# Kernel optimization log

Hardware: AMD Instinct MI355X
Metric: run time of the kernel (lower is better)

Reference implementation:

```python
import jax, jax.numpy as jnp
import numpy as np

D = 1024  # d_model

def setup_inputs() -> dict:
    key = jax.random.key(0)
    ks = jax.random.split(key, 12)
    s = 1.0 / np.sqrt(D)  # torch Linear default init scale
    inp = {
        "q": jax.random.normal(ks[0], (4, 4096, D), dtype=jnp.float32),
        "k": jax.random.normal(ks[1], (4, 4096, D), dtype=jnp.float32),
        "v": jax.random.normal(ks[2], (4, 4096, D), dtype=jnp.float32),
        "Wq": jax.random.uniform(ks[3], (D, D), jnp.float32, -s, s),
        "bq": jax.random.uniform(ks[4], (D,), jnp.float32, -s, s),
        "Wk": jax.random.uniform(ks[5], (D, D), jnp.float32, -s, s),
        "bk": jax.random.uniform(ks[6], (D,), jnp.float32, -s, s),
        "Wv": jax.random.uniform(ks[7], (D, D), jnp.float32, -s, s),
        "bv": jax.random.uniform(ks[8], (D,), jnp.float32, -s, s),
        "Wo": jax.random.uniform(ks[9], (D, D), jnp.float32, -s, s),
        "bo": jax.random.uniform(ks[10], (D,), jnp.float32, -s, s),
    }
    return inp

def reference(q, k, v, Wq, bq, Wk, bk, Wv, bv, Wo, bo):
    # phi feature map: exp(-x^2 / 2)
    phi = lambda x: jnp.exp(-0.5 * x * x)
    Q = phi(q @ Wq.T + bq)            # [B, N, D]
    K = phi(k @ Wk.T + bk)            # [B, N, D]
    V = v @ Wv.T + bv                 # [B, N, D]
    # linear attention: aggregate K^T V once, then contract with Q
    KV = jnp.einsum('bnd,bnl->bdl', K, V)                 # [B, D, D]
    Z = 1.0 / (jnp.einsum('bnd,bd->bn', Q, K.sum(axis=1)) + 1e-6)  # [B, N]
    out = jnp.einsum('bnd,bdl->bnl', Q, KV) * Z[..., None]         # [B, N, D]
    return out @ Wo.T + bo
```

## Files before the change

kernel.cpp:

```cpp
#include <hip/hip_runtime.h>

typedef unsigned short u16;
typedef unsigned int u32;
typedef unsigned long long u64;

typedef __attribute__((ext_vector_type(8))) short short8;
typedef __attribute__((ext_vector_type(4))) float floatx4;

__device__ __forceinline__ float b2f(u16 h) {
  u32 u = ((u32)h) << 16;
  return __builtin_bit_cast(float, u);
}
__device__ __forceinline__ u16 f2b(float f) {
  u32 u = __builtin_bit_cast(u32, f);
  u32 r = 0x7FFFu + ((u >> 16) & 1u);
  return (u16)((u + r) >> 16);
}

__device__ __forceinline__ void gl_lds16(const void* g, void* l) {
  __builtin_amdgcn_global_load_lds(
      (__attribute__((address_space(1))) void*)(u64)g,
      (__attribute__((address_space(3))) void*)(u32)(u64)l, 16, 0, 0);
}

enum { EPI_PHI_BIAS = 0, EPI_BIAS = 1, EPI_NONE = 2,
       EPI_ZBIAS_F32 = 3 };

template<int EPI, bool TRANS_OUT>
__global__ __launch_bounds__(512, 2)
void gemm_bt256(const u16* __restrict__ Ap, const u16* __restrict__ Bp0,
                const float* __restrict__ bias, const float* __restrict__ Zall,
                void* __restrict__ Cp,
                int M, int N, int K, int ldA, int ldB, int ldC,
                long sAb, long sBb, long sCb, long sZb, int abmask, int kshift)
{
  constexpr int TSTRIDE = 65536;
  constexpr int BOFF    = 32768;
  __shared__ char smem[2 * TSTRIDE];

  const int tid  = threadIdx.x;
  const int lane = tid & 63;
  const int wave = tid >> 6;
  const int wm = wave >> 2, wn = wave & 3;
  const int fl = lane & 15;
  const int q  = lane >> 4;
  const int r4 = q * 4;
  const int bm0 = blockIdx.x * 256, bn0 = blockIdx.y * 256;
  const int bz = blockIdx.z;
  const int abz = bz & abmask;
  const int kbase = (bz >> kshift) * K;

  const u16* Ah = Ap  + (size_t)abz * sAb + kbase;
  const u16* Bh = Bp0 + (size_t)abz * sBb + kbase;

  const u16* gA[4]; const u16* gB[4]; int sL[4];
  #pragma unroll
  for (int n = 0; n < 4; ++n) {
    int j = n * 512 + tid;
    int R = j >> 3, c = (j & 7) ^ (R & 7);
    gA[n] = Ah + (size_t)(bm0 + R) * ldA + c * 8;
    gB[n] = Bh + (size_t)(bn0 + R) * ldB + c * 8;
    sL[n] = (n * 512 + wave * 64) * 16;
  }

  int aoff[8], boff[4];
  #pragma unroll
  for (int i = 0; i < 8; ++i) {
    int ra = wm * 128 + i * 16 + fl;
    aoff[i] = ra * 128 + ((q ^ (ra & 7)) * 16);
  }
  #pragma unroll
  for (int i = 0; i < 4; ++i) {
    int rb = wn * 64 + i * 16 + fl;
    boff[i] = rb * 128 + ((q ^ (rb & 7)) * 16);
  }

  floatx4 zero = {0.f, 0.f, 0.f, 0.f};
  floatx4 acc[8][4];
  #pragma unroll
  for (int i = 0; i < 8; ++i)
    #pragma unroll
    for (int j = 0; j < 4; ++j) acc[i][j] = zero;

  auto stA = [&](int t, int n) {
    gl_lds16(gA[n] + t * 64, smem + (t & 1) * TSTRIDE + sL[n]);
  };
  auto stB = [&](int t, int n) {
    gl_lds16(gB[n] + t * 64, smem + (t & 1) * TSTRIDE + BOFF + sL[n]);
  };

  const int NT = K >> 6;
  #pragma unroll
  for (int n = 0; n < 4; ++n) stA(0, n);
  #pragma unroll
  for (int n = 0; n < 4; ++n) stB(0, n);
  if (NT > 1) {
    stA(1, 0); stA(1, 2); stB(1, 0); stB(1, 1); stA(1, 1); stA(1, 3);
    asm volatile("s_waitcnt vmcnt(6)\ns_barrier" ::: "memory");
  } else {
    asm volatile("s_waitcnt vmcnt(0)\ns_barrier" ::: "memory");
  }

  for (int u = 0; u < NT; ++u) {
    const bool pf1 = u + 1 < NT;
    const bool pf2 = u + 2 < NT;
    const char* bufc = smem + (u & 1) * TSTRIDE;
    short8 aL[8], aH[8], b01[4], b23[4];

    #pragma unroll
    for (int i = 0; i < 4; ++i) {
      aL[2 * i]     = *(const short8*)(bufc + aoff[i]);
      aL[2 * i + 1] = *(const short8*)(bufc + (aoff[i] ^ 64));
    }
    #pragma unroll
    for (int i = 0; i < 2; ++i) {
      b01[2 * i]     = *(const short8*)(bufc + BOFF + boff[i]);
      b01[2 * i + 1] = *(const short8*)(bufc + BOFF + (boff[i] ^ 64));
    }
    if (pf1) { stB(u + 1, 2); stB(u + 1, 3); }
    __builtin_amdgcn_s_barrier();
    asm volatile("s_waitcnt lgkmcnt(0)" ::: "memory");
    __builtin_amdgcn_sched_barrier(0);
    __builtin_amdgcn_s_setprio(1);
    #pragma unroll
    for (int kk = 0; kk < 2; ++kk)
      #pragma unroll
      for (int mi = 0; mi < 4; ++mi)
        #pragma unroll
        for (int ni = 0; ni < 2; ++ni)
          acc[mi][ni] = __builtin_amdgcn_mfma_f32_16x16x32_bf16(
              aL[2 * mi + kk], b01[2 * ni + kk], acc[mi][ni], 0, 0, 0);
    __builtin_amdgcn_s_setprio(0);
    __builtin_amdgcn_s_barrier();

    #pragma unroll
    for (int i = 0; i < 2; ++i) {
      b23[2 * i]     = *(const short8*)(bufc + BOFF + boff[i + 2]);
      b23[2 * i + 1] = *(const short8*)(bufc + BOFF + (boff[i + 2] ^ 64));
    }
    if (pf2) { stA(u + 2, 0); stA(u + 2, 2); }
    __builtin_amdgcn_s_barrier();
    asm volatile("s_waitcnt lgkmcnt(0)" ::: "memory");
    __builtin_amdgcn_sched_barrier(0);
    __builtin_amdgcn_s_setprio(1);
    #pragma unroll
    for (int kk = 0; kk < 2; ++kk)
      #pragma unroll
      for (int mi = 0; mi < 4; ++mi)
        #pragma unroll
        for (int ni = 0; ni < 2; ++ni)
          acc[mi][ni + 2] = __builtin_amdgcn_mfma_f32_16x16x32_bf16(
              aL[2 * mi + kk], b23[2 * ni + kk], acc[mi][ni + 2], 0, 0, 0);
    __builtin_amdgcn_s_setprio(0);
    __builtin_amdgcn_s_barrier();

    #pragma unroll
    for (int i = 0; i < 4; ++i) {
      aH[2 * i]     = *(const short8*)(bufc + aoff[i + 4]);
      aH[2 * i + 1] = *(const short8*)(bufc + (aoff[i + 4] ^ 64));
    }
    if (pf2) { stB(u + 2, 0); stB(u + 2, 1); }
    __builtin_amdgcn_s_barrier();
    asm volatile("s_waitcnt lgkmcnt(0)" ::: "memory");
    __builtin_amdgcn_sched_barrier(0);
    __builtin_amdgcn_s_setprio(1);
    #pragma unroll
    for (int kk = 0; kk < 2; ++kk)
      #pragma unroll
      for (int mi = 0; mi < 4; ++mi)
        #pragma unroll
        for (int ni = 0; ni < 2; ++ni)
          acc[mi + 4][ni + 2] = __builtin_amdgcn_mfma_f32_16x16x32_bf16(
              aH[2 * mi + kk], b23[2 * ni + kk], acc[mi + 4][ni + 2], 0, 0, 0);
    __builtin_amdgcn_s_setprio(0);
    __builtin_amdgcn_s_barrier();

    if (pf2) { stA(u + 2, 1); stA(u + 2, 3); }
    __builtin_amdgcn_s_setprio(1);
    #pragma unroll
    for (int kk = 0; kk < 2; ++kk)
      #pragma unroll
      for (int mi = 0; mi < 4; ++mi)
        #pragma unroll
        for (int ni = 0; ni < 2; ++ni)
          acc[mi + 4][ni] = __builtin_amdgcn_mfma_f32_16x16x32_bf16(
              aH[2 * mi + kk], b01[2 * ni + kk], acc[mi + 4][ni], 0, 0, 0);
    __builtin_amdgcn_s_setprio(0);
    if (pf1) {
      if (pf2) asm volatile("s_waitcnt vmcnt(6) lgkmcnt(0)\ns_barrier" ::: "memory");
      else     asm volatile("s_waitcnt vmcnt(0) lgkmcnt(0)\ns_barrier" ::: "memory");
    }
  }

  if constexpr (!TRANS_OUT) {
    #pragma unroll
    for (int mi = 0; mi < 8; ++mi) {
      #pragma unroll
      for (int ni = 0; ni < 4; ++ni) {
        int col = bn0 + wn * 64 + ni * 16 + fl;
        #pragma unroll
        for (int r = 0; r < 4; ++r) {
          int row = bm0 + wm * 128 + mi * 16 + r4 + r;
          float vv = acc[mi][ni][r];
          if constexpr (EPI == EPI_PHI_BIAS) {
            vv += bias[col];
            vv = __expf(-0.5f * vv * vv);
          }
          if constexpr (EPI == EPI_ZBIAS_F32)
            vv = vv * Zall[(size_t)abz * sZb + row] + bias[col];
          if constexpr (EPI == EPI_ZBIAS_F32)
            ((float*)Cp)[(size_t)bz * sCb + (size_t)row * ldC + col] = vv;
          else
            ((u16*)Cp)[(size_t)bz * sCb + (size_t)row * ldC + col] = f2b(vv);
        }
      }
    }
  } else {
    u16* sT = (u16*)smem;
    #pragma unroll
    for (int p = 0; p < 2; ++p) {
      __syncthreads();
      if ((wn >> 1) == p) {
        #pragma unroll
        for (int mi = 0; mi < 8; ++mi) {
          #pragma unroll
          for (int ni = 0; ni < 4; ++ni) {
            int colL = wn * 64 + ni * 16 + fl;
            int row0 = wm * 128 + mi * 16 + r4;
            float bcol = bias[bn0 + colL];
            ushort4 h;
            #pragma unroll
            for (int r = 0; r < 4; ++r) {
              float vv = acc[mi][ni][r] + bcol;
              if constexpr (EPI == EPI_PHI_BIAS) vv = __expf(-0.5f * vv * vv);
              ((u16*)&h)[r] = f2b(vv);
            }
            *(ushort4*)(sT + (colL - p * 128) * 264 + row0) = h;
          }
        }
      }
      __syncthreads();
      #pragma unroll
      for (int i = 0; i < 8; ++i) {
        int c = tid + i * 512;
        int dloc = c >> 5, t8 = (c & 31) * 8;
        int4 vv = *(const int4*)(sT + dloc * 264 + t8);
        int gd = bn0 + p * 128 + dloc;
        int gt = bm0 + t8;
        int batch = gt >> 12, tt = gt & 4095;
        *(int4*)((u16*)Cp + ((size_t)batch * N + gd) * 4096 + tt) = vv;
      }
    }
  }
}

__global__ __launch_bounds__(256)
void fcvt(const float* __restrict__ src, u16* __restrict__ dst) {
  size_t i = ((size_t)blockIdx.x * 256 + threadIdx.x) * 8;
  float4 a = *(const float4*)(src + i);
  float4 b = *(const float4*)(src + i + 4);
  union { ushort4 h[2]; int4 v; } o;
  o.h[0].x = f2b(a.x); o.h[0].y = f2b(a.y); o.h[0].z = f2b(a.z); o.h[0].w = f2b(a.w);
  o.h[1].x = f2b(b.x); o.h[1].y = f2b(b.y); o.h[1].z = f2b(b.z); o.h[1].w = f2b(b.w);
  *(int4*)(dst + i) = o.v;
}

__global__ __launch_bounds__(256)
void wconv(const float* __restrict__ w0, const float* __restrict__ w1,
           const float* __restrict__ w2, const float* __restrict__ w3,
           u16* __restrict__ dst) {
  unsigned e = blockIdx.x * 256 + threadIdx.x;
  int mat = e >> 18;
  size_t off = (size_t)(e & 262143) * 4;
  const float* src = mat == 0 ? w0 : mat == 1 ? w1 : mat == 2 ? w2 : w3;
  float4 v = *(const float4*)(src + off);
  ushort4 h;
  h.x = f2b(v.x); h.y = f2b(v.y); h.z = f2b(v.z); h.w = f2b(v.w);
  *(ushort4*)(dst + (size_t)mat * 1048576 + off) = h;
}

__global__ __launch_bounds__(256)
void reduce4(const u16* __restrict__ P, u16* __restrict__ out) {
  size_t i = ((size_t)blockIdx.x * 256 + threadIdx.x) * 8;
  int4 a = *(const int4*)(P + i);
  int4 b = *(const int4*)(P + i + 4194304);
  int4 c = *(const int4*)(P + i + 8388608);
  int4 d = *(const int4*)(P + i + 12582912);
  const u16* ha = (const u16*)&a; const u16* hb = (const u16*)&b;
  const u16* hc = (const u16*)&c; const u16* hd = (const u16*)&d;
  ushort4 o0, o1;
  #pragma unroll
  for (int j = 0; j < 8; ++j) {
    float s = b2f(ha[j]) + b2f(hb[j]) + b2f(hc[j]) + b2f(hd[j]);
    ((u16*)(j < 4 ? &o0 : &o1))[j & 3] = f2b(s);
  }
  *(ushort4*)(out + i) = o0;
  *(ushort4*)(out + i + 4) = o1;
}

__global__ __launch_bounds__(256)
void ksum_rows(const u16* __restrict__ KT, float* __restrict__ Ksum) {
  int lane = threadIdx.x & 63;
  int row = blockIdx.x * 4 + (threadIdx.x >> 6);
  const u16* p = KT + (size_t)row * 4096;
  float s = 0.f;
  #pragma unroll
  for (int i = 0; i < 8; ++i) {
    int4 d = *(const int4*)(p + i * 512 + lane * 8);
    const u16* h = (const u16*)&d;
    #pragma unroll
    for (int j = 0; j < 8; ++j) s += b2f(h[j]);
  }
  #pragma unroll
  for (int off = 32; off; off >>= 1) s += __shfl_xor(s, off, 64);
  if (lane == 0) Ksum[row] = s;
}

__global__ __launch_bounds__(256)
void zden(const u16* __restrict__ Qb, const float* __restrict__ Ksum,
          float* __restrict__ Z) {
  int lane = threadIdx.x & 63;
  int t = blockIdx.x * 4 + (threadIdx.x >> 6);
  const u16* qp = Qb + (size_t)t * 1024;
  const float* ks = Ksum + (size_t)(t >> 12) * 1024;
  float s = 0.f;
  #pragma unroll
  for (int i = 0; i < 2; ++i) {
    int idx = i * 512 + lane * 8;
    int4 d = *(const int4*)(qp + idx);
    const u16* h = (const u16*)&d;
    float4 k0 = *(const float4*)(ks + idx);
    float4 k1 = *(const float4*)(ks + idx + 4);
    s += b2f(h[0]) * k0.x + b2f(h[1]) * k0.y + b2f(h[2]) * k0.z + b2f(h[3]) * k0.w
       + b2f(h[4]) * k1.x + b2f(h[5]) * k1.y + b2f(h[6]) * k1.z + b2f(h[7]) * k1.w;
  }
  #pragma unroll
  for (int off = 32; off; off >>= 1) s += __shfl_xor(s, off, 64);
  if (lane == 0) Z[t] = 1.0f / (s + 1e-6f);
}

extern "C" void kernel_launch(void* const* d_in, const int* in_sizes, int n_in,
                              void* d_out, int out_size, void* d_ws, size_t ws_size,
                              hipStream_t stream) {
  const float* q  = (const float*)d_in[0];
  const float* k  = (const float*)d_in[1];
  const float* v  = (const float*)d_in[2];
  const float* Wq = (const float*)d_in[3];
  const float* bq = (const float*)d_in[4];
  const float* Wk = (const float*)d_in[5];
  const float* bk = (const float*)d_in[6];
  const float* Wv = (const float*)d_in[7];
  const float* bv = (const float*)d_in[8];
  const float* Wo = (const float*)d_in[9];
  const float* bo = (const float*)d_in[10];
  float* out = (float*)d_out;

  u16* Wqb = (u16*)d_ws;
  u16* Wkb = Wqb + 1048576;
  u16* Wvb = Wkb + 1048576;
  u16* Wob = Wvb + 1048576;
  u16* Qb  = Wob + 1048576;
  u16* KT  = Qb  + 16777216;
  u16* VT  = KT  + 16777216;
  u16* KVr = VT  + 16777216;
  float* Ksum = (float*)(KVr + 4194304);
  float* Z    = Ksum + 4096;
  u16* kb16 = Qb;
  u16* vb16 = Qb;
  u16* Pkv  = Qb;
  u16* Pg   = VT;
  u16* Gp   = KT;
  u16* qb16 = VT;

  wconv<<<4096, 256, 0, stream>>>(Wq, Wk, Wv, Wo, Wqb);
  fcvt<<<8192, 256, 0, stream>>>(k, kb16);

  dim3 gp(64, 4, 1);
  gemm_bt256<EPI_PHI_BIAS, true><<<gp, 512, 0, stream>>>(
      kb16, Wkb, bk, nullptr, KT, 16384, 1024, 1024, 1024, 1024, 0,
      0, 0, 0, 0, 0, 2);
  ksum_rows<<<1024, 256, 0, stream>>>(KT, Ksum);

  fcvt<<<8192, 256, 0, stream>>>(v, vb16);
  gemm_bt256<EPI_BIAS, true><<<gp, 512, 0, stream>>>(
      vb16, Wvb, bv, nullptr, VT, 16384, 1024, 1024, 1024, 1024, 0,
      0, 0, 0, 0, 0, 2);

  dim3 g2(4, 4, 16);
  gemm_bt256<EPI_NONE, false><<<g2, 512, 0, stream>>>(
      KT, VT, nullptr, nullptr, Pkv, 1024, 1024, 1024, 4096, 4096, 1024,
      4194304L, 4194304L, 1048576L, 0, 3, 2);
  reduce4<<<2048, 256, 0, stream>>>(Pkv, KVr);

  dim3 gg(4, 4, 16);
  gemm_bt256<EPI_NONE, false><<<gg, 512, 0, stream>>>(
      Wob, KVr, nullptr, nullptr, Pg, 1024, 1024, 256, 1024, 1024, 1024,
      0L, 1048576L, 1048576L, 0, 3, 2);
  reduce4<<<2048, 256, 0, stream>>>(Pg, Gp);

  fcvt<<<8192, 256, 0, stream>>>(q, qb16);
  gemm_bt256<EPI_PHI_BIAS, false><<<gp, 512, 0, stream>>>(
      qb16, Wqb, bq, nullptr, Qb, 16384, 1024, 1024, 1024, 1024, 1024,
      0, 0, 0, 0, 0, 2);
  zden<<<4096, 256, 0, stream>>>(Qb, Ksum, Z);

  dim3 gf(16, 4, 4);
  gemm_bt256<EPI_ZBIAS_F32, false><<<gf, 512, 0, stream>>>(
      Qb, Gp, bo, Z, out, 4096, 1024, 1024, 1024, 1024, 1024,
      4194304L, 1048576L, 4194304L, 4096L, 3, 2);
}
```

Measured before the change: 302.8 us.

## Prefetch next K-tile LDS fragments at loop tail and drop intermediate barriers

Restructures the double-buffered GEMM main loop so that the next tile's aL and b01 fragments are read from LDS at the end of the current iteration. The remaining fragment reads (b23, aH) move earlier in each iteration. This removes several s_barrier plus lgkmcnt(0) wait points per K-step, aiming to overlap LDS reads with MFMA work. The global-to-LDS prefetch schedule and vmcnt thresholds change to match. The cost is fewer synchronisation points between LDS reads and async global_load_lds writes into the same buffer, which risks races and needs more live registers.

```diff
diff --git a/kernel.cpp b/kernel.cpp
--- a/kernel.cpp
+++ b/kernel.cpp
@@ -95,32 +95,38 @@
   #pragma unroll
   for (int n = 0; n < 4; ++n) stB(0, n);
   if (NT > 1) {
-    stA(1, 0); stA(1, 2); stB(1, 0); stB(1, 1); stA(1, 1); stA(1, 3);
-    asm volatile("s_waitcnt vmcnt(6)\ns_barrier" ::: "memory");
+    stA(1, 0); stA(1, 2);
+    stB(1, 0); stB(1, 1); stB(1, 2); stB(1, 3);
+    asm volatile("s_waitcnt vmcnt(6)" ::: "memory");
   } else {
-    asm volatile("s_waitcnt vmcnt(0)\ns_barrier" ::: "memory");
+    asm volatile("s_waitcnt vmcnt(0)" ::: "memory");
+  }
+  __builtin_amdgcn_s_barrier();
+
+  short8 aL[8], aH[8], b01[4], b23[4];
+  #pragma unroll
+  for (int i = 0; i < 4; ++i) {
+    aL[2 * i]     = *(const short8*)(smem + aoff[i]);
+    aL[2 * i + 1] = *(const short8*)(smem + (aoff[i] ^ 64));
+  }
+  #pragma unroll
+  for (int i = 0; i < 2; ++i) {
+    b01[2 * i]     = *(const short8*)(smem + BOFF + boff[i]);
+    b01[2 * i + 1] = *(const short8*)(smem + BOFF + (boff[i] ^ 64));
   }
 
   for (int u = 0; u < NT; ++u) {
     const bool pf1 = u + 1 < NT;
     const bool pf2 = u + 2 < NT;
     const char* bufc = smem + (u & 1) * TSTRIDE;
-    short8 aL[8], aH[8], b01[4], b23[4];
-
-    #pragma unroll
-    for (int i = 0; i < 4; ++i) {
-      aL[2 * i]     = *(const short8*)(bufc + aoff[i]);
-      aL[2 * i + 1] = *(const short8*)(bufc + (aoff[i] ^ 64));
+    const char* bufn = smem + ((u + 1) & 1) * TSTRIDE;
+
+    #pragma unroll
+    for (int i = 0; i < 2; ++i) {
+      b23[2 * i]     = *(const short8*)(bufc + BOFF + boff[i + 2]);
+      b23[2 * i + 1] = *(const short8*)(bufc + BOFF + (boff[i + 2] ^ 64));
     }
-    #pragma unroll
-    for (int i = 0; i < 2; ++i) {
-      b01[2 * i]     = *(const short8*)(bufc + BOFF + boff[i]);
-      b01[2 * i + 1] = *(const short8*)(bufc + BOFF + (boff[i] ^ 64));
-    }
-    if (pf1) { stB(u + 1, 2); stB(u + 1, 3); }
-    __builtin_amdgcn_s_barrier();
-    asm volatile("s_waitcnt lgkmcnt(0)" ::: "memory");
-    __builtin_amdgcn_sched_barrier(0);
+    if (pf1) { stA(u + 1, 1); stA(u + 1, 3); }
     __builtin_amdgcn_s_setprio(1);
     #pragma unroll
     for (int kk = 0; kk < 2; ++kk)
@@ -134,14 +140,11 @@
     __builtin_amdgcn_s_barrier();
 
     #pragma unroll
-    for (int i = 0; i < 2; ++i) {
-      b23[2 * i]     = *(const short8*)(bufc + BOFF + boff[i + 2]);
-      b23[2 * i + 1] = *(const short8*)(bufc + BOFF + (boff[i + 2] ^ 64));
+    for (int i = 0; i < 4; ++i) {
+      aH[2 * i]     = *(const short8*)(bufc + aoff[i + 4]);
+      aH[2 * i + 1] = *(const short8*)(bufc + (aoff[i + 4] ^ 64));
     }
     if (pf2) { stA(u + 2, 0); stA(u + 2, 2); }
-    __builtin_amdgcn_s_barrier();
-    asm volatile("s_waitcnt lgkmcnt(0)" ::: "memory");
-    __builtin_amdgcn_sched_barrier(0);
     __builtin_amdgcn_s_setprio(1);
     #pragma unroll
     for (int kk = 0; kk < 2; ++kk)
@@ -154,15 +157,7 @@
     __builtin_amdgcn_s_setprio(0);
     __builtin_amdgcn_s_barrier();
 
-    #pragma unroll
-    for (int i = 0; i < 4; ++i) {
-      aH[2 * i]     = *(const short8*)(bufc + aoff[i + 4]);
-      aH[2 * i + 1] = *(const short8*)(bufc + (aoff[i + 4] ^ 64));
-    }
     if (pf2) { stB(u + 2, 0); stB(u + 2, 1); }
-    __builtin_amdgcn_s_barrier();
-    asm volatile("s_waitcnt lgkmcnt(0)" ::: "memory");
-    __builtin_amdgcn_sched_barrier(0);
     __builtin_amdgcn_s_setprio(1);
     #pragma unroll
     for (int kk = 0; kk < 2; ++kk)
@@ -173,9 +168,7 @@
           acc[mi + 4][ni + 2] = __builtin_amdgcn_mfma_f32_16x16x32_bf16(
               aH[2 * mi + kk], b23[2 * ni + kk], acc[mi + 4][ni + 2], 0, 0, 0);
     __builtin_amdgcn_s_setprio(0);
-    __builtin_amdgcn_s_barrier();
-
-    if (pf2) { stA(u + 2, 1); stA(u + 2, 3); }
+
     __builtin_amdgcn_s_setprio(1);
     #pragma unroll
     for (int kk = 0; kk < 2; ++kk)
@@ -187,8 +180,20 @@
               aH[2 * mi + kk], b01[2 * ni + kk], acc[mi + 4][ni], 0, 0, 0);
     __builtin_amdgcn_s_setprio(0);
     if (pf1) {
-      if (pf2) asm volatile("s_waitcnt vmcnt(6) lgkmcnt(0)\ns_barrier" ::: "memory");
-      else     asm volatile("s_waitcnt vmcnt(0) lgkmcnt(0)\ns_barrier" ::: "memory");
+      if (pf2) asm volatile("s_waitcnt vmcnt(4)" ::: "memory");
+      else     asm volatile("s_waitcnt vmcnt(0)" ::: "memory");
+      #pragma unroll
+      for (int i = 0; i < 4; ++i) {
+        aL[2 * i]     = *(const short8*)(bufn + aoff[i]);
+        aL[2 * i + 1] = *(const short8*)(bufn + (aoff[i] ^ 64));
+      }
+      #pragma unroll
+      for (int i = 0; i < 2; ++i) {
+        b01[2 * i]     = *(const short8*)(bufn + BOFF + boff[i]);
+        b01[2 * i + 1] = *(const short8*)(bufn + BOFF + (boff[i] ^ 64));
+      }
+      if (pf2) { stB(u + 2, 2); stB(u + 2, 3); }
+      __builtin_amdgcn_s_barrier();
     }
   }
 
```

After: 318.0 us. 5.0% more time.
